# Performance work log

Measured on AMD Instinct MI355X. Metric: run time of the kernel, lower is better.

## Reference

```python
import jax, jax.numpy as jnp
import numpy as np

B, H, W, C = 2, 256, 256, 192
HEADS, WIN, SHIFT = 6, 8, 4
HID = 4 * C
N = WIN * WIN            # tokens per window
HD = C // HEADS
SCALE = HD ** -0.5

# ---- static relative-position index (matches torch buffer construction) ----
_c = np.stack(np.meshgrid(np.arange(WIN), np.arange(WIN), indexing='ij')).reshape(2, -1)
_r = (_c[:, :, None] - _c[:, None, :]).transpose(1, 2, 0)
_r[..., 0] += WIN - 1
_r[..., 1] += WIN - 1
_r[..., 0] *= 2 * WIN - 1
RPI = _r.sum(-1)  # [N, N]

# ---- static shift attention mask (Swin-style region mask, shift_size>0) ----
def _build_shift_mask():
    m = np.zeros((H, W))
    cnt = 0
    sl = (slice(0, -WIN), slice(-WIN, -SHIFT), slice(-SHIFT, None))
    for hs in sl:
        for ws in sl:
            m[hs, ws] = cnt
            cnt += 1
    mw = m.reshape(H // WIN, WIN, W // WIN, WIN).transpose(0, 2, 1, 3).reshape(-1, N)
    am = mw[:, None, :] - mw[:, :, None]  # unsqueeze(1) - unsqueeze(2)
    return jnp.asarray(np.where(am != 0, -100.0, 0.0), jnp.float32)  # [nW, N, N]

ATTN_MASK = _build_shift_mask()

def _win_part(x):  # [B,H,W,c] -> [B*nW, N, c]
    b, c = x.shape[0], x.shape[-1]
    x = x.reshape(b, H // WIN, WIN, W // WIN, WIN, c).transpose(0, 1, 3, 2, 4, 5)
    return x.reshape(-1, N, c)

def _win_rev(w):  # [B*nW, N, c] -> [B,H,W,c]
    c = w.shape[-1]
    x = w.reshape(-1, H // WIN, W // WIN, WIN, WIN, c).transpose(0, 1, 3, 2, 4, 5)
    return x.reshape(-1, H, W, c)

def _ln(x, w, b):
    mu = x.mean(-1, keepdims=True)
    v = ((x - mu) ** 2).mean(-1, keepdims=True)
    return (x - mu) / jnp.sqrt(v + 1e-5) * w + b


def setup_inputs() -> dict:
    key = jax.random.key(0)
    ks = jax.random.split(key, 9)
    s = jnp.float32(0.02)
    f32 = jnp.float32
    return {
        'x': jax.random.normal(ks[0], (B, H * W, C), f32),
        'norm1_w': jnp.ones((C,), f32), 'norm1_b': jnp.zeros((C,), f32),
        'q_w': jax.random.normal(ks[1], (C, C), f32) * s, 'q_b': jnp.zeros((C,), f32),
        'kv_w': jax.random.normal(ks[2], (C, 2 * C), f32) * s, 'kv_b': jnp.zeros((2 * C,), f32),
        'rpb': jax.random.normal(ks[3], ((2 * WIN - 1) ** 2, HEADS), f32) * s,
        'proj_w': jax.random.normal(ks[4], (C, C), f32) * s, 'proj_b': jnp.zeros((C,), f32),
        'norm2_w': jnp.ones((C,), f32), 'norm2_b': jnp.zeros((C,), f32),
        'l1_w': jax.random.normal(ks[5], (C, HID), f32) * s, 'l1_b': jnp.zeros((HID,), f32),
        'dw_w': jax.random.normal(ks[6], (3, 3, 1, HID), f32) * s, 'dw_b': jnp.zeros((HID,), f32),
        'l2_w': jax.random.normal(ks[7], (HID, C), f32) * s, 'l2_b': jnp.zeros((C,), f32),
    }


def reference(x, norm1_w, norm1_b, q_w, q_b, kv_w, kv_b, rpb, proj_w, proj_b,
              norm2_w, norm2_b, l1_w, l1_b, dw_w, dw_b, l2_w, l2_b):
    shortcut = x
    xn = _ln(x, norm1_w, norm1_b)
    q = (xn @ q_w + q_b).reshape(B, H, W, C)
    kv = (xn @ kv_w + kv_b).reshape(B, H, W, 2 * C)
    # cyclic shift
    q = jnp.roll(q, (-SHIFT, -SHIFT), axis=(1, 2))
    kv = jnp.roll(kv, (-SHIFT, -SHIFT), axis=(1, 2))
    # window partition -> heads
    qw = _win_part(q).reshape(-1, N, HEADS, HD).transpose(0, 2, 1, 3)          # [B_,h,N,hd]
    kvw = _win_part(kv).reshape(-1, N, 2, HEADS, HD).transpose(2, 0, 3, 1, 4)
    kw, vw = kvw[0], kvw[1]
    attn = jnp.einsum('bhnd,bhmd->bhnm', qw * SCALE, kw)                       # [B_,h,N,N]
    bias = rpb[RPI.reshape(-1)].reshape(N, N, HEADS).transpose(2, 0, 1)        # [h,N,N]
    attn = attn + bias[None]
    nW = ATTN_MASK.shape[0]
    attn = attn.reshape(B, nW, HEADS, N, N) + ATTN_MASK[None, :, None]
    attn = jax.nn.softmax(attn.reshape(-1, HEADS, N, N), axis=-1)
    y = jnp.einsum('bhnm,bhmd->bnhd', attn, vw).reshape(-1, N, C)
    y = y @ proj_w + proj_b
    xa = _win_rev(y)
    xa = jnp.roll(xa, (SHIFT, SHIFT), axis=(1, 2)).reshape(B, H * W, C)
    x = shortcut + xa
    # LeFF: linear -> GELU -> 3x3 depthwise conv -> GELU -> linear
    xn = _ln(x, norm2_w, norm2_b)
    h = jax.nn.gelu(xn @ l1_w + l1_b, approximate=False).reshape(B, H, W, HID)
    h = jax.lax.conv_general_dilated(h, dw_w, (1, 1), 'SAME',
                                     dimension_numbers=('NHWC', 'HWIO', 'NHWC'),
                                     feature_group_count=HID) + dw_b
    h = jax.nn.gelu(h, approximate=False).reshape(B, H * W, HID)
    return x + (h @ l2_w + l2_b)
```

## Files before the change

kernel.cpp:

```cpp
#include <hip/hip_runtime.h>
#include <math.h>

typedef float f32x4 __attribute__((ext_vector_type(4)));
typedef short bf16x8 __attribute__((ext_vector_type(8)));
typedef short bf16x4 __attribute__((ext_vector_type(4)));

__device__ __forceinline__ short f2bf(float f) {
  unsigned u = __builtin_bit_cast(unsigned, f);
  u = (u + 0x7FFFu + ((u >> 16) & 1u)) >> 16;
  return (short)u;
}
__device__ __forceinline__ float bf2f(short s) {
  unsigned u = ((unsigned)(unsigned short)s) << 16;
  return __builtin_bit_cast(float, u);
}
__device__ __forceinline__ float gelu_exact(float x) {
  return 0.5f * x * (1.0f + erff(x * 0.70710678118654752f));
}
__device__ __forceinline__ void gld16(const short* g, short* l) {
  __builtin_amdgcn_global_load_lds(
      (const __attribute__((address_space(1))) void*)g,
      (__attribute__((address_space(3))) void*)l, 16, 0, 0);
}

__device__ __forceinline__ long perm_row(int b, int ho, int wo) {
  int hs = (ho + 252) & 255, ws = (wo + 252) & 255;
  int w = ((hs >> 3) << 5) | (ws >> 3);
  int t = ((hs & 7) << 3) | (ws & 7);
  return ((long)b << 16) | (w << 6) | t;
}
__device__ __forceinline__ long unperm_row(long m) {
  int b = (int)(m >> 16);
  int w = ((int)m >> 6) & 1023, t = (int)m & 63;
  int hs = ((w >> 5) << 3) | (t >> 3);
  int ws = ((w & 31) << 3) | (t & 7);
  int ho = (hs + 4) & 255, wo = (ws + 4) & 255;
  return ((long)b << 16) | (ho << 8) | wo;
}

__global__ __launch_bounds__(256) void ln1_kernel(const float* __restrict__ x,
                                                  const float* __restrict__ w,
                                                  const float* __restrict__ b,
                                                  short* __restrict__ out) {
  int lane = threadIdx.x & 63;
  long row = (long)blockIdx.x * 4 + (threadIdx.x >> 6);
  const float* xr = x + row * 192;
  float v0 = xr[lane], v1 = xr[lane + 64], v2 = xr[lane + 128];
  float s = v0 + v1 + v2, s2 = v0 * v0 + v1 * v1 + v2 * v2;
#pragma unroll
  for (int m = 1; m < 64; m <<= 1) {
    s += __shfl_xor(s, m);
    s2 += __shfl_xor(s2, m);
  }
  float mu = s * (1.0f / 192.0f);
  float rstd = rsqrtf(s2 * (1.0f / 192.0f) - mu * mu + 1e-5f);
  long drow = perm_row((int)(row >> 16), ((int)row >> 8) & 255, (int)row & 255);
  short* o = out + drow * 192;
  o[lane] = f2bf((v0 - mu) * rstd * w[lane] + b[lane]);
  o[lane + 64] = f2bf((v1 - mu) * rstd * w[lane + 64] + b[lane + 64]);
  o[lane + 128] = f2bf((v2 - mu) * rstd * w[lane + 128] + b[lane + 128]);
}

__global__ __launch_bounds__(256) void ln2_kernel(const short* __restrict__ x,
                                                  const float* __restrict__ w,
                                                  const float* __restrict__ b,
                                                  short* __restrict__ out) {
  int lane = threadIdx.x & 63;
  long row = (long)blockIdx.x * 4 + (threadIdx.x >> 6);
  const short* xr = x + row * 192;
  float v0 = bf2f(xr[lane]), v1 = bf2f(xr[lane + 64]), v2 = bf2f(xr[lane + 128]);
  float s = v0 + v1 + v2, s2 = v0 * v0 + v1 * v1 + v2 * v2;
#pragma unroll
  for (int m = 1; m < 64; m <<= 1) {
    s += __shfl_xor(s, m);
    s2 += __shfl_xor(s2, m);
  }
  float mu = s * (1.0f / 192.0f);
  float rstd = rsqrtf(s2 * (1.0f / 192.0f) - mu * mu + 1e-5f);
  short* o = out + row * 192;
  o[lane] = f2bf((v0 - mu) * rstd * w[lane] + b[lane]);
  o[lane + 64] = f2bf((v1 - mu) * rstd * w[lane + 64] + b[lane + 64]);
  o[lane + 128] = f2bf((v2 - mu) * rstd * w[lane + 128] + b[lane + 128]);
}

__global__ __launch_bounds__(256) void wprep_kernel(const float* __restrict__ w,
                                                    short* __restrict__ bt,
                                                    int K, int N) {
  long i = (long)blockIdx.x * 256 + threadIdx.x;
  if (i >= (long)K * N) return;
  int n = (int)(i / K), k = (int)(i % K);
  bt[i] = f2bf(w[(long)k * N + n]);
}

__global__ __launch_bounds__(256) void bias_prep(const float* __restrict__ rpb,
                                                 float* __restrict__ biasTab) {
  int i = blockIdx.x * 256 + threadIdx.x;
  int k = i & 63, q = (i >> 6) & 63, h = i >> 12;
  int dr = (q >> 3) - (k >> 3) + 7;
  int dc = (q & 7) - (k & 7) + 7;
  biasTab[i] = rpb[(dr * 15 + dc) * 6 + h] * 1.4426950408889634f;
}

__global__ __launch_bounds__(384) void fused_attn_kernel(
    const short* __restrict__ xn, const short* __restrict__ bt1,
    const short* __restrict__ bt2, const float* __restrict__ q_b,
    const float* __restrict__ kv_b, const float* __restrict__ proj_b,
    const float* __restrict__ residf, const float* __restrict__ biasTab,
    short* __restrict__ x2bf) {
  __shared__ short S_[57344];
  const int tid = threadIdx.x;
  const int lane = tid & 63, wid = tid >> 6;
  const int lr = lane & 15, lg = lane >> 4;
  const int bid = blockIdx.x;
  const int wglob = (bid & 7) * 256 + (bid >> 3);
  const int w = wglob & 1023;
  const int wr = w >> 5, wc = w & 31;
  const long wbase = (long)wglob * 64;
  const int RB = 12800 + wid * 7424;

#pragma unroll
  for (int p = 0; p < 4; ++p) {
    int g = p * 384 + tid;
    int r = g / 24, c = g % 24;
    *(float4*)(&S_[r * 200 + c * 8]) =
        *(const float4*)(xn + (wbase + r) * 192 + c * 8);
  }
  __syncthreads();

  {
    f32x4 acc[4][6] = {};
#pragma unroll
    for (int ks = 0; ks < 6; ++ks) {
      bf16x8 a[4], b[6];
#pragma unroll
      for (int mf = 0; mf < 4; ++mf)
        a[mf] = *(const bf16x8*)(&S_[(mf * 16 + lr) * 200 + ks * 32 + lg * 8]);
#pragma unroll
      for (int st = 0; st < 3; ++st)
#pragma unroll
        for (int nf = 0; nf < 2; ++nf)
          b[st * 2 + nf] = *(const bf16x8*)(
              bt1 + (long)(st * 192 + wid * 32 + nf * 16 + lr) * 192 +
              ks * 32 + lg * 8);
#pragma unroll
      for (int mf = 0; mf < 4; ++mf)
#pragma unroll
        for (int j = 0; j < 6; ++j)
          acc[mf][j] = __builtin_amdgcn_mfma_f32_16x16x32_bf16(
              a[mf], b[j], acc[mf][j], 0, 0, 0);
    }
#pragma unroll
    for (int mf = 0; mf < 4; ++mf) {
      int row0 = mf * 16 + lg * 4;
#pragma unroll
      for (int nf = 0; nf < 2; ++nf) {
        int c = nf * 16 + lr;
        float qb = q_b[wid * 32 + c];
        float kb = kv_b[wid * 32 + c];
        float vb = kv_b[192 + wid * 32 + c];
#pragma unroll
        for (int r = 0; r < 4; ++r) {
          S_[RB + (row0 + r) * 40 + c] = f2bf(acc[mf][nf][r] + qb);
          S_[RB + 2560 + (row0 + r) * 40 + c] = f2bf(acc[mf][2 + nf][r] + kb);
        }
        bf16x4 vv;
#pragma unroll
        for (int r = 0; r < 4; ++r) vv[r] = f2bf(acc[mf][4 + nf][r] + vb);
        *(bf16x4*)(&S_[RB + 5120 + c * 72 + row0]) = vv;
      }
    }
  }

  bf16x8 aq[4], bk[4];
#pragma unroll
  for (int i = 0; i < 4; ++i) {
    aq[i] = *(const bf16x8*)(&S_[RB + (i * 16 + lr) * 40 + lg * 8]);
    bk[i] = *(const bf16x8*)(&S_[RB + 2560 + (i * 16 + lr) * 40 + lg * 8]);
  }
  f32x4 s[4][4] = {};
#pragma unroll
  for (int mi = 0; mi < 4; ++mi)
#pragma unroll
    for (int ni = 0; ni < 4; ++ni)
      s[mi][ni] = __builtin_amdgcn_mfma_f32_16x16x32_bf16(aq[mi], bk[ni],
                                                          s[mi][ni], 0, 0, 0);

  const float SCL2 = 0.17677669529663687f * 1.4426950408889634f;
  const float MASKC = -144.26950408889634f;
  const bool edge = (wr == 31) || (wc == 31);
  int ridk[4] = {0, 0, 0, 0};
  if (edge) {
#pragma unroll
    for (int ni = 0; ni < 4; ++ni) {
      int k = ni * 16 + lr;
      int kh = wr * 8 + (k >> 3), kw = wc * 8 + (k & 7);
      ridk[ni] = 3 * ((kh < 248) ? 0 : ((kh < 252) ? 1 : 2)) +
                 ((kw < 248) ? 0 : ((kw < 252) ? 1 : 2));
    }
  }
  float rinv[4][4];
#pragma unroll
  for (int mi = 0; mi < 4; ++mi) {
#pragma unroll
    for (int r = 0; r < 4; ++r) {
      int q = mi * 16 + lg * 4 + r;
      const float* bp = biasTab + (wid << 12) + (q << 6);
      int ridq = 0;
      if (edge) {
        int qh = wr * 8 + (q >> 3), qw = wc * 8 + (q & 7);
        ridq = 3 * ((qh < 248) ? 0 : ((qh < 252) ? 1 : 2)) +
               ((qw < 248) ? 0 : ((qw < 252) ? 1 : 2));
      }
      float lv[4];
      float mx = -1e30f;
#pragma unroll
      for (int ni = 0; ni < 4; ++ni) {
        float lvv = s[mi][ni][r] * SCL2 + bp[ni * 16 + lr];
        if (edge && ridq != ridk[ni]) lvv += MASKC;
        lv[ni] = lvv;
        mx = fmaxf(mx, lvv);
      }
#pragma unroll
      for (int m = 1; m < 16; m <<= 1) mx = fmaxf(mx, __shfl_xor(mx, m));
      float sum = 0.0f;
#pragma unroll
      for (int ni = 0; ni < 4; ++ni) {
        float p = exp2f(lv[ni] - mx);
        lv[ni] = p;
        sum += p;
      }
#pragma unroll
      for (int m = 1; m < 16; m <<= 1) sum += __shfl_xor(sum, m);
      rinv[mi][r] = 1.0f / sum;
#pragma unroll
      for (int ni = 0; ni < 4; ++ni)
        S_[RB + q * 72 + ni * 16 + lr] = f2bf(lv[ni]);
    }
  }

  f32x4 o[4][2] = {};
#pragma unroll
  for (int ks = 0; ks < 2; ++ks) {
    bf16x8 ap[4], bv[2];
#pragma unroll
    for (int mi = 0; mi < 4; ++mi)
      ap[mi] = *(const bf16x8*)(&S_[RB + (mi * 16 + lr) * 72 + ks * 32 +
                                    lg * 8]);
#pragma unroll
    for (int ni = 0; ni < 2; ++ni)
      bv[ni] = *(const bf16x8*)(&S_[RB + 5120 + (ni * 16 + lr) * 72 +
                                    ks * 32 + lg * 8]);
#pragma unroll
    for (int mi = 0; mi < 4; ++mi)
#pragma unroll
      for (int ni = 0; ni < 2; ++ni)
        o[mi][ni] = __builtin_amdgcn_mfma_f32_16x16x32_bf16(ap[mi], bv[ni],
                                                            o[mi][ni], 0, 0, 0);
  }
#pragma unroll
  for (int mi = 0; mi < 4; ++mi)
#pragma unroll
    for (int r = 0; r < 4; ++r) {
      int q = mi * 16 + lg * 4 + r;
      float ri = rinv[mi][r];
#pragma unroll
      for (int ni = 0; ni < 2; ++ni)
        S_[RB + q * 40 + ni * 16 + lr] = f2bf(o[mi][ni][r] * ri);
    }
  __syncthreads();

  {
    f32x4 acc[4][2] = {};
#pragma unroll
    for (int ks = 0; ks < 6; ++ks) {
      bf16x8 a[4], bq[2];
#pragma unroll
      for (int mf = 0; mf < 4; ++mf)
        a[mf] = *(const bf16x8*)(&S_[12800 + ks * 7424 +
                                     (mf * 16 + lr) * 40 + lg * 8]);
#pragma unroll
      for (int nf = 0; nf < 2; ++nf)
        bq[nf] = *(const bf16x8*)(bt2 +
                                  (long)(wid * 32 + nf * 16 + lr) * 192 +
                                  ks * 32 + lg * 8);
#pragma unroll
      for (int mf = 0; mf < 4; ++mf)
#pragma unroll
        for (int nf = 0; nf < 2; ++nf)
          acc[mf][nf] = __builtin_amdgcn_mfma_f32_16x16x32_bf16(
              a[mf], bq[nf], acc[mf][nf], 0, 0, 0);
    }
#pragma unroll
    for (int mf = 0; mf < 4; ++mf)
#pragma unroll
      for (int nf = 0; nf < 2; ++nf) {
        int n = wid * 32 + nf * 16 + lr;
#pragma unroll
        for (int r = 0; r < 4; ++r) {
          long m = wbase + mf * 16 + lg * 4 + r;
          long oidx = unperm_row(m) * 192 + n;
          x2bf[oidx] = f2bf(acc[mf][nf][r] + proj_b[n] + residf[oidx]);
        }
      }
  }
}

template <int NTOT, int EPI>
__global__ __launch_bounds__(256) void gemm1_kernel(
    const short* __restrict__ A, const short* __restrict__ Bt,
    const float* __restrict__ B0, short* __restrict__ outp,
    int nblk, int mgx, int iters, int mtiles) {
  __shared__ short As[128 * 192];
  const int tid = threadIdx.x;
  const int lane = tid & 63, wid = tid >> 6;
  const int lr = lane & 15, lg = lane >> 4;
  const int xcd = blockIdx.x & 7;
  const int i = blockIdx.x >> 3;
  const int n0 = (i % nblk) * 64;
  const int mg = xcd * mgx + i / nblk;

  bf16x8 bf[6][4];
#pragma unroll
  for (int ks = 0; ks < 6; ++ks)
#pragma unroll
    for (int ni = 0; ni < 4; ++ni)
      bf[ks][ni] = *(const bf16x8*)(Bt + (long)(n0 + ni * 16 + lr) * 192 +
                                    ks * 32 + lg * 8);

  int src_s[12];
#pragma unroll
  for (int s = 0; s < 12; ++s) {
    int lo = (wid * 12 + s) * 1024 + lane * 16;
    int r = lo / 384, c = lo % 384;
    src_s[s] = r * 192 + ((c ^ ((r & 7) << 4)) >> 1);
  }
  const int xorv = (lr & 7) << 4;

#pragma unroll 1
  for (int it = 0; it < iters; ++it) {
    int mt = mg * iters + it;
    if (mt >= mtiles) continue;
    long m0 = (long)mt * 128;
    const short* Ab = A + m0 * 192;
    __syncthreads();
#pragma unroll
    for (int s = 0; s < 12; ++s)
      gld16(Ab + src_s[s], As + (wid * 12 + s) * 512);
    __syncthreads();
    f32x4 acc[2][4] = {};
#pragma unroll
    for (int ks = 0; ks < 6; ++ks) {
      const char* asb = (const char*)As;
      const int col = (ks * 64 + lg * 16) ^ xorv;
      bf16x8 a0 = *(const bf16x8*)(asb + (wid * 32 + lr) * 384 + col);
      bf16x8 a1 = *(const bf16x8*)(asb + (wid * 32 + 16 + lr) * 384 + col);
#pragma unroll
      for (int ni = 0; ni < 4; ++ni) {
        acc[0][ni] = __builtin_amdgcn_mfma_f32_16x16x32_bf16(a0, bf[ks][ni],
                                                             acc[0][ni], 0, 0, 0);
        acc[1][ni] = __builtin_amdgcn_mfma_f32_16x16x32_bf16(a1, bf[ks][ni],
                                                             acc[1][ni], 0, 0, 0);
      }
    }
#pragma unroll
    for (int mi = 0; mi < 2; ++mi) {
#pragma unroll
      for (int ni = 0; ni < 4; ++ni) {
        int n = n0 + ni * 16 + lr;
        long rowb = m0 + wid * 32 + mi * 16 + lg * 4;
#pragma unroll
        for (int r = 0; r < 4; ++r) {
          long m = rowb + r;
          outp[m * NTOT + n] = f2bf(gelu_exact(acc[mi][ni][r] + B0[n]));
        }
      }
    }
  }
}

__global__ __launch_bounds__(256) void dwconv_kernel(const short* __restrict__ hbc,
                                                     const float* __restrict__ dww,
                                                     const float* __restrict__ dwb,
                                                     short* __restrict__ h2c,
                                                     int yh) {
  int t = blockIdx.x * 256 + threadIdx.x;
  int cg = t % 96;
  int px = t / 96;
  int strip = blockIdx.y;

  float wv[9][8];
#pragma unroll
  for (int tap = 0; tap < 9; ++tap) {
    float4 a = *(const float4*)(dww + tap * 768 + cg * 8);
    float4 b = *(const float4*)(dww + tap * 768 + cg * 8 + 4);
    wv[tap][0] = a.x; wv[tap][1] = a.y; wv[tap][2] = a.z; wv[tap][3] = a.w;
    wv[tap][4] = b.x; wv[tap][5] = b.y; wv[tap][6] = b.z; wv[tap][7] = b.w;
  }
  float bias[8];
  {
    float4 a = *(const float4*)(dwb + cg * 8);
    float4 b = *(const float4*)(dwb + cg * 8 + 4);
    bias[0] = a.x; bias[1] = a.y; bias[2] = a.z; bias[3] = a.w;
    bias[4] = b.x; bias[5] = b.y; bias[6] = b.z; bias[7] = b.w;
  }

#pragma unroll 2
  for (int pp = 0; pp < 16; ++pp) {
    int py = strip * 16 + pp;
    int ybase = yh * 128 + py;
    float acc[8];
#pragma unroll
    for (int j = 0; j < 8; ++j) acc[j] = bias[j];
#pragma unroll
    for (int dy = 0; dy < 3; ++dy) {
      int yy = ybase + dy - 1;
      if (yy < 0 || yy > 255) continue;
#pragma unroll
      for (int dx = 0; dx < 3; ++dx) {
        int xx = px + dx - 1;
        if (xx < 0 || xx > 255) continue;
        bf16x8 hv = *(const bf16x8*)(hbc + ((long)yy * 256 + xx) * 768 + cg * 8);
#pragma unroll
        for (int j = 0; j < 8; ++j) acc[j] += bf2f(hv[j]) * wv[dy * 3 + dx][j];
      }
    }
    bf16x8 ov;
#pragma unroll
    for (int j = 0; j < 8; ++j) ov[j] = f2bf(gelu_exact(acc[j]));
    *(bf16x8*)(h2c + ((long)py * 256 + px) * 768 + cg * 8) = ov;
  }
}

__global__ __launch_bounds__(256) void gemm2_kernel(
    const short* __restrict__ A, const short* __restrict__ Bt,
    const float* __restrict__ bias, const short* __restrict__ residb,
    float* __restrict__ outp) {
  __shared__ short As[64][72];
  __shared__ short Bs[192][72];
  const int tid = threadIdx.x;
  const int lane = tid & 63, wid = tid >> 6;
  const int lr = lane & 15, lg = lane >> 4;
  const int wm = wid >> 1, wn = wid & 1;
  const int wg = (blockIdx.x & 7) * 64 + (blockIdx.x >> 3);
  const long m0 = (long)wg * 64;

  f32x4 acc[2][6] = {};
#pragma unroll 1
  for (int kc = 0; kc < 12; ++kc) {
    __syncthreads();
#pragma unroll
    for (int p = 0; p < 2; ++p) {
      int g = p * 256 + tid;
      int r = g >> 3, c = g & 7;
      *(float4*)(&As[r][c * 8]) =
          *(const float4*)(A + (m0 + r) * 768 + kc * 64 + c * 8);
    }
#pragma unroll
    for (int p = 0; p < 6; ++p) {
      int g = p * 256 + tid;
      int n = g >> 3, c = g & 7;
      *(float4*)(&Bs[n][c * 8]) =
          *(const float4*)(Bt + (long)n * 768 + kc * 64 + c * 8);
    }
    __syncthreads();
#pragma unroll
    for (int ks = 0; ks < 2; ++ks) {
      bf16x8 a[2], b[6];
#pragma unroll
      for (int mf = 0; mf < 2; ++mf)
        a[mf] = *(const bf16x8*)(&As[wm * 32 + mf * 16 + lr][ks * 32 + lg * 8]);
#pragma unroll
      for (int nf = 0; nf < 6; ++nf)
        b[nf] = *(const bf16x8*)(&Bs[wn * 96 + nf * 16 + lr][ks * 32 + lg * 8]);
#pragma unroll
      for (int mf = 0; mf < 2; ++mf)
#pragma unroll
        for (int nf = 0; nf < 6; ++nf)
          acc[mf][nf] = __builtin_amdgcn_mfma_f32_16x16x32_bf16(
              a[mf], b[nf], acc[mf][nf], 0, 0, 0);
    }
  }
#pragma unroll
  for (int mf = 0; mf < 2; ++mf)
#pragma unroll
    for (int nf = 0; nf < 6; ++nf) {
      int n = wn * 96 + nf * 16 + lr;
      long rowb = m0 + wm * 32 + mf * 16 + lg * 4;
#pragma unroll
      for (int r = 0; r < 4; ++r) {
        long idx = (rowb + r) * 192 + n;
        outp[idx] = acc[mf][nf][r] + bias[n] + bf2f(residb[idx]);
      }
    }
}

extern "C" void kernel_launch(void* const* d_in, const int* in_sizes, int n_in,
                              void* d_out, int out_size, void* d_ws, size_t ws_size,
                              hipStream_t stream) {
  const float* x = (const float*)d_in[0];
  const float* n1w = (const float*)d_in[1];
  const float* n1b = (const float*)d_in[2];
  const float* q_w = (const float*)d_in[3];
  const float* q_b = (const float*)d_in[4];
  const float* kv_w = (const float*)d_in[5];
  const float* kv_b = (const float*)d_in[6];
  const float* rpb = (const float*)d_in[7];
  const float* proj_w = (const float*)d_in[8];
  const float* proj_b = (const float*)d_in[9];
  const float* n2w = (const float*)d_in[10];
  const float* n2b = (const float*)d_in[11];
  const float* l1_w = (const float*)d_in[12];
  const float* l1_b = (const float*)d_in[13];
  const float* dw_w = (const float*)d_in[14];
  const float* dw_b = (const float*)d_in[15];
  const float* l2_w = (const float*)d_in[16];
  const float* l2_b = (const float*)d_in[17];
  float* out = (float*)d_out;

  char* ws = (char*)d_ws;
  short* xn = (short*)ws;
  short* hbc = (short*)(ws + 50331648);
  short* h2c = (short*)(ws + 150994944);
  short* x2bf = (short*)(ws + 201326592);
  short* bt1 = (short*)(ws + 251658240);
  short* bt2 = bt1 + 110592;
  short* bt3 = bt2 + 36864;
  short* bt4 = bt3 + 147456;
  float* biasTab = (float*)(ws + 252542976);
  short* xn2 = xn;

  wprep_kernel<<<144, 256, 0, stream>>>(q_w, bt1, 192, 192);
  wprep_kernel<<<288, 256, 0, stream>>>(kv_w, bt1 + 36864, 192, 384);
  wprep_kernel<<<144, 256, 0, stream>>>(proj_w, bt2, 192, 192);
  wprep_kernel<<<576, 256, 0, stream>>>(l1_w, bt3, 192, 768);
  wprep_kernel<<<576, 256, 0, stream>>>(l2_w, bt4, 768, 192);
  bias_prep<<<96, 256, 0, stream>>>(rpb, biasTab);

  ln1_kernel<<<32768, 256, 0, stream>>>(x, n1w, n1b, xn);
  fused_attn_kernel<<<2048, 384, 0, stream>>>(xn, bt1, bt2, q_b, kv_b, proj_b,
                                              x, biasTab, x2bf);
  ln2_kernel<<<32768, 256, 0, stream>>>(x2bf, n2w, n2b, xn2);

  for (int b = 0; b < 2; ++b) {
    long toff = (long)b * 65536 * 192;
    gemm1_kernel<768, 2><<<1536, 256, 0, stream>>>(
        xn2 + toff, bt3, l1_b, hbc, 12, 16, 4, 512);
    for (int yh = 0; yh < 2; ++yh) {
      long ooff = ((long)b * 65536 + (long)yh * 32768) * 192;
      dwconv_kernel<<<dim3(96, 8), 256, 0, stream>>>(hbc, dw_w, dw_b, h2c, yh);
      gemm2_kernel<<<512, 256, 0, stream>>>(h2c, bt4, l2_b, x2bf + ooff,
                                            out + ooff);
    }
  }
}
```

Baseline: 732.2 us.

## Split attention work across two waves per head and load activations directly

The fused window-attention kernel moves from 6 waves (one per head) to 12 waves: two per head, each owning half the query rows and half the per-head QKV output columns. The projection GEMM is split over 12 waves of 16 columns each. The shared-memory staging of the input tile is dropped, and A fragments are read straight from global memory. This is meant to raise occupancy and latency hiding. In exchange it adds an extra block barrier, larger LDS use per block, and repeated global reads of xn by every wave.

Result: slower. 759.9 us (+3.8%).

```diff
diff --git a/kernel.cpp b/kernel.cpp
--- a/kernel.cpp
+++ b/kernel.cpp
@@ -101,85 +101,75 @@
   biasTab[i] = rpb[(dr * 15 + dc) * 6 + h] * 1.4426950408889634f;
 }
 
-__global__ __launch_bounds__(384) void fused_attn_kernel(
+__global__ __launch_bounds__(768, 3) void fused_attn_kernel(
     const short* __restrict__ xn, const short* __restrict__ bt1,
     const short* __restrict__ bt2, const float* __restrict__ q_b,
     const float* __restrict__ kv_b, const float* __restrict__ proj_b,
     const float* __restrict__ residf, const float* __restrict__ biasTab,
     short* __restrict__ x2bf) {
-  __shared__ short S_[57344];
+  __shared__ short S_[72192];
   const int tid = threadIdx.x;
   const int lane = tid & 63, wid = tid >> 6;
+  const int h = wid >> 1, ha = wid & 1;
   const int lr = lane & 15, lg = lane >> 4;
   const int bid = blockIdx.x;
   const int wglob = (bid & 7) * 256 + (bid >> 3);
   const int w = wglob & 1023;
   const int wr = w >> 5, wc = w & 31;
   const long wbase = (long)wglob * 64;
-  const int RB = 12800 + wid * 7424;
-
-#pragma unroll
-  for (int p = 0; p < 4; ++p) {
-    int g = p * 384 + tid;
-    int r = g / 24, c = g % 24;
-    *(float4*)(&S_[r * 200 + c * 8]) =
-        *(const float4*)(xn + (wbase + r) * 192 + c * 8);
-  }
-  __syncthreads();
+  const int RB = h * 12032;
+  const int cb = h * 32 + ha * 16;
 
   {
-    f32x4 acc[4][6] = {};
+    f32x4 acc[4][3] = {};
 #pragma unroll
     for (int ks = 0; ks < 6; ++ks) {
-      bf16x8 a[4], b[6];
+      bf16x8 a[4], b[3];
 #pragma unroll
       for (int mf = 0; mf < 4; ++mf)
-        a[mf] = *(const bf16x8*)(&S_[(mf * 16 + lr) * 200 + ks * 32 + lg * 8]);
+        a[mf] = *(const bf16x8*)(xn + (wbase + mf * 16 + lr) * 192 +
+                                 ks * 32 + lg * 8);
 #pragma unroll
       for (int st = 0; st < 3; ++st)
-#pragma unroll
-        for (int nf = 0; nf < 2; ++nf)
-          b[st * 2 + nf] = *(const bf16x8*)(
-              bt1 + (long)(st * 192 + wid * 32 + nf * 16 + lr) * 192 +
-              ks * 32 + lg * 8);
+        b[st] = *(const bf16x8*)(bt1 + (long)(st * 192 + cb + lr) * 192 +
+                                 ks * 32 + lg * 8);
 #pragma unroll
       for (int mf = 0; mf < 4; ++mf)
 #pragma unroll
-        for (int j = 0; j < 6; ++j)
-          acc[mf][j] = __builtin_amdgcn_mfma_f32_16x16x32_bf16(
-              a[mf], b[j], acc[mf][j], 0, 0, 0);
-    }
+        for (int st = 0; st < 3; ++st)
+          acc[mf][st] = __builtin_amdgcn_mfma_f32_16x16x32_bf16(
+              a[mf], b[st], acc[mf][st], 0, 0, 0);
+    }
+    const int c2 = ha * 16 + lr;
+    const float qb = q_b[cb + lr];
+    const float kb = kv_b[cb + lr];
+    const float vb = kv_b[192 + cb + lr];
 #pragma unroll
     for (int mf = 0; mf < 4; ++mf) {
       int row0 = mf * 16 + lg * 4;
 #pragma unroll
-      for (int nf = 0; nf < 2; ++nf) {
-        int c = nf * 16 + lr;
-        float qb = q_b[wid * 32 + c];
-        float kb = kv_b[wid * 32 + c];
-        float vb = kv_b[192 + wid * 32 + c];
-#pragma unroll
-        for (int r = 0; r < 4; ++r) {
-          S_[RB + (row0 + r) * 40 + c] = f2bf(acc[mf][nf][r] + qb);
-          S_[RB + 2560 + (row0 + r) * 40 + c] = f2bf(acc[mf][2 + nf][r] + kb);
-        }
-        bf16x4 vv;
-#pragma unroll
-        for (int r = 0; r < 4; ++r) vv[r] = f2bf(acc[mf][4 + nf][r] + vb);
-        *(bf16x4*)(&S_[RB + 5120 + c * 72 + row0]) = vv;
-      }
-    }
-  }
-
-  bf16x8 aq[4], bk[4];
-#pragma unroll
-  for (int i = 0; i < 4; ++i) {
-    aq[i] = *(const bf16x8*)(&S_[RB + (i * 16 + lr) * 40 + lg * 8]);
+      for (int r = 0; r < 4; ++r) {
+        S_[RB + (row0 + r) * 40 + c2] = f2bf(acc[mf][0][r] + qb);
+        S_[RB + 2560 + (row0 + r) * 40 + c2] = f2bf(acc[mf][1][r] + kb);
+      }
+      bf16x4 vv;
+#pragma unroll
+      for (int r = 0; r < 4; ++r) vv[r] = f2bf(acc[mf][2][r] + vb);
+      *(bf16x4*)(&S_[RB + 5120 + c2 * 72 + row0]) = vv;
+    }
+  }
+  __syncthreads();
+
+  bf16x8 aq[2], bk[4];
+#pragma unroll
+  for (int i = 0; i < 2; ++i)
+    aq[i] = *(const bf16x8*)(&S_[RB + (ha * 32 + i * 16 + lr) * 40 + lg * 8]);
+#pragma unroll
+  for (int i = 0; i < 4; ++i)
     bk[i] = *(const bf16x8*)(&S_[RB + 2560 + (i * 16 + lr) * 40 + lg * 8]);
-  }
-  f32x4 s[4][4] = {};
-#pragma unroll
-  for (int mi = 0; mi < 4; ++mi)
+  f32x4 s[2][4] = {};
+#pragma unroll
+  for (int mi = 0; mi < 2; ++mi)
 #pragma unroll
     for (int ni = 0; ni < 4; ++ni)
       s[mi][ni] = __builtin_amdgcn_mfma_f32_16x16x32_bf16(aq[mi], bk[ni],
@@ -198,13 +188,13 @@
                  ((kw < 248) ? 0 : ((kw < 252) ? 1 : 2));
     }
   }
-  float rinv[4][4];
-#pragma unroll
-  for (int mi = 0; mi < 4; ++mi) {
+  float rinv[2][4];
+#pragma unroll
+  for (int mi = 0; mi < 2; ++mi) {
 #pragma unroll
     for (int r = 0; r < 4; ++r) {
-      int q = mi * 16 + lg * 4 + r;
-      const float* bp = biasTab + (wid << 12) + (q << 6);
+      int q = ha * 32 + mi * 16 + lg * 4 + r;
+      const float* bp = biasTab + (h << 12) + (q << 6);
       int ridq = 0;
       if (edge) {
         int qh = wr * 8 + (q >> 3), qw = wc * 8 + (q & 7);
@@ -234,34 +224,35 @@
       rinv[mi][r] = 1.0f / sum;
 #pragma unroll
       for (int ni = 0; ni < 4; ++ni)
-        S_[RB + q * 72 + ni * 16 + lr] = f2bf(lv[ni]);
-    }
-  }
-
-  f32x4 o[4][2] = {};
+        S_[RB + 7424 + q * 72 + ni * 16 + lr] = f2bf(lv[ni]);
+    }
+  }
+
+  f32x4 o[2][2] = {};
 #pragma unroll
   for (int ks = 0; ks < 2; ++ks) {
-    bf16x8 ap[4], bv[2];
-#pragma unroll
-    for (int mi = 0; mi < 4; ++mi)
-      ap[mi] = *(const bf16x8*)(&S_[RB + (mi * 16 + lr) * 72 + ks * 32 +
-                                    lg * 8]);
+    bf16x8 ap[2], bv[2];
+#pragma unroll
+    for (int mi = 0; mi < 2; ++mi)
+      ap[mi] = *(const bf16x8*)(&S_[RB + 7424 +
+                                    (ha * 32 + mi * 16 + lr) * 72 +
+                                    ks * 32 + lg * 8]);
 #pragma unroll
     for (int ni = 0; ni < 2; ++ni)
       bv[ni] = *(const bf16x8*)(&S_[RB + 5120 + (ni * 16 + lr) * 72 +
                                     ks * 32 + lg * 8]);
 #pragma unroll
-    for (int mi = 0; mi < 4; ++mi)
+    for (int mi = 0; mi < 2; ++mi)
 #pragma unroll
       for (int ni = 0; ni < 2; ++ni)
         o[mi][ni] = __builtin_amdgcn_mfma_f32_16x16x32_bf16(ap[mi], bv[ni],
                                                             o[mi][ni], 0, 0, 0);
   }
 #pragma unroll
-  for (int mi = 0; mi < 4; ++mi)
+  for (int mi = 0; mi < 2; ++mi)
 #pragma unroll
     for (int r = 0; r < 4; ++r) {
-      int q = mi * 16 + lg * 4 + r;
+      int q = ha * 32 + mi * 16 + lg * 4 + r;
       float ri = rinv[mi][r];
 #pragma unroll
       for (int ni = 0; ni < 2; ++ni)
@@ -270,37 +261,29 @@
   __syncthreads();
 
   {
-    f32x4 acc[4][2] = {};
+    f32x4 acc[4] = {};
 #pragma unroll
     for (int ks = 0; ks < 6; ++ks) {
-      bf16x8 a[4], bq[2];
+      bf16x8 a[4], bq;
 #pragma unroll
       for (int mf = 0; mf < 4; ++mf)
-        a[mf] = *(const bf16x8*)(&S_[12800 + ks * 7424 +
-                                     (mf * 16 + lr) * 40 + lg * 8]);
-#pragma unroll
-      for (int nf = 0; nf < 2; ++nf)
-        bq[nf] = *(const bf16x8*)(bt2 +
-                                  (long)(wid * 32 + nf * 16 + lr) * 192 +
-                                  ks * 32 + lg * 8);
+        a[mf] = *(const bf16x8*)(&S_[ks * 12032 + (mf * 16 + lr) * 40 +
+                                     lg * 8]);
+      bq = *(const bf16x8*)(bt2 + (long)(wid * 16 + lr) * 192 + ks * 32 +
+                            lg * 8);
 #pragma unroll
       for (int mf = 0; mf < 4; ++mf)
-#pragma unroll
-        for (int nf = 0; nf < 2; ++nf)
-          acc[mf][nf] = __builtin_amdgcn_mfma_f32_16x16x32_bf16(
-              a[mf], bq[nf], acc[mf][nf], 0, 0, 0);
-    }
+        acc[mf] = __builtin_amdgcn_mfma_f32_16x16x32_bf16(a[mf], bq, acc[mf],
+                                                          0, 0, 0);
+    }
+    int n = wid * 16 + lr;
 #pragma unroll
     for (int mf = 0; mf < 4; ++mf)
 #pragma unroll
-      for (int nf = 0; nf < 2; ++nf) {
-        int n = wid * 32 + nf * 16 + lr;
-#pragma unroll
-        for (int r = 0; r < 4; ++r) {
-          long m = wbase + mf * 16 + lg * 4 + r;
-          long oidx = unperm_row(m) * 192 + n;
-          x2bf[oidx] = f2bf(acc[mf][nf][r] + proj_b[n] + residf[oidx]);
-        }
+      for (int r = 0; r < 4; ++r) {
+        long m = wbase + mf * 16 + lg * 4 + r;
+        long oidx = unperm_row(m) * 192 + n;
+        x2bf[oidx] = f2bf(acc[mf][r] + proj_b[n] + residf[oidx]);
       }
   }
 }
@@ -537,7 +520,7 @@
   bias_prep<<<96, 256, 0, stream>>>(rpb, biasTab);
 
   ln1_kernel<<<32768, 256, 0, stream>>>(x, n1w, n1b, xn);
-  fused_attn_kernel<<<2048, 384, 0, stream>>>(xn, bt1, bt2, q_b, kv_b, proj_b,
+  fused_attn_kernel<<<2048, 768, 0, stream>>>(xn, bt1, bt2, q_b, kv_b, proj_b,
                                               x, biasTab, x2bf);
   ln2_kernel<<<32768, 256, 0, stream>>>(x2bf, n2w, n2b, xn2);
 
```

## Make attention kernel persistent over 8 windows with async double-buffered loads

Applied to the files above, without the earlier changes.

The fused attention kernel now runs 256 blocks, each looping over 8 consecutive windows. The next window's normalized input is staged into swizzled LDS through global_load_lds double buffering, and the K/V weight fragments are held in registers across iterations. The residual add and un-permutation move out of the attention epilogue into ln2, which reads the window-ordered output with a gather and writes both x2bf and the normalized tensor. This removes scattered residual reads from the attention kernel and reuses weights across windows. In exchange it needs more LDS and registers, which may lower occupancy, and leaves only 256 blocks to fill the GPU.

After: 862.3 us. +17.8%, slower.

```diff
diff --git a/kernel.cpp b/kernel.cpp
--- a/kernel.cpp
+++ b/kernel.cpp
@@ -28,14 +28,6 @@
   int w = ((hs >> 3) << 5) | (ws >> 3);
   int t = ((hs & 7) << 3) | (ws & 7);
   return ((long)b << 16) | (w << 6) | t;
-}
-__device__ __forceinline__ long unperm_row(long m) {
-  int b = (int)(m >> 16);
-  int w = ((int)m >> 6) & 1023, t = (int)m & 63;
-  int hs = ((w >> 5) << 3) | (t >> 3);
-  int ws = ((w & 31) << 3) | (t & 7);
-  int ho = (hs + 4) & 255, wo = (ws + 4) & 255;
-  return ((long)b << 16) | (ho << 8) | wo;
 }
 
 __global__ __launch_bounds__(256) void ln1_kernel(const float* __restrict__ x,
@@ -61,14 +53,24 @@
   o[lane + 128] = f2bf((v2 - mu) * rstd * w[lane + 128] + b[lane + 128]);
 }
 
-__global__ __launch_bounds__(256) void ln2_kernel(const short* __restrict__ x,
+__global__ __launch_bounds__(256) void ln2_kernel(const float* __restrict__ x,
+                                                  const short* __restrict__ yw,
                                                   const float* __restrict__ w,
                                                   const float* __restrict__ b,
-                                                  short* __restrict__ out) {
+                                                  short* __restrict__ xn2,
+                                                  short* __restrict__ x2bf) {
   int lane = threadIdx.x & 63;
   long row = (long)blockIdx.x * 4 + (threadIdx.x >> 6);
-  const short* xr = x + row * 192;
-  float v0 = bf2f(xr[lane]), v1 = bf2f(xr[lane + 64]), v2 = bf2f(xr[lane + 128]);
+  long drow = perm_row((int)(row >> 16), ((int)row >> 8) & 255, (int)row & 255);
+  const float* xr = x + row * 192;
+  const short* yr = yw + drow * 192;
+  float v0 = xr[lane] + bf2f(yr[lane]);
+  float v1 = xr[lane + 64] + bf2f(yr[lane + 64]);
+  float v2 = xr[lane + 128] + bf2f(yr[lane + 128]);
+  short* xo = x2bf + row * 192;
+  xo[lane] = f2bf(v0);
+  xo[lane + 64] = f2bf(v1);
+  xo[lane + 128] = f2bf(v2);
   float s = v0 + v1 + v2, s2 = v0 * v0 + v1 * v1 + v2 * v2;
 #pragma unroll
   for (int m = 1; m < 64; m <<= 1) {
@@ -77,7 +79,7 @@
   }
   float mu = s * (1.0f / 192.0f);
   float rstd = rsqrtf(s2 * (1.0f / 192.0f) - mu * mu + 1e-5f);
-  short* o = out + row * 192;
+  short* o = xn2 + row * 192;
   o[lane] = f2bf((v0 - mu) * rstd * w[lane] + b[lane]);
   o[lane + 64] = f2bf((v1 - mu) * rstd * w[lane + 64] + b[lane + 64]);
   o[lane + 128] = f2bf((v2 - mu) * rstd * w[lane + 128] + b[lane + 128]);
@@ -105,203 +107,237 @@
     const short* __restrict__ xn, const short* __restrict__ bt1,
     const short* __restrict__ bt2, const float* __restrict__ q_b,
     const float* __restrict__ kv_b, const float* __restrict__ proj_b,
-    const float* __restrict__ residf, const float* __restrict__ biasTab,
-    short* __restrict__ x2bf) {
-  __shared__ short S_[57344];
+    const float* __restrict__ biasTab, short* __restrict__ yw) {
+  __shared__ short S_[69120];
   const int tid = threadIdx.x;
   const int lane = tid & 63, wid = tid >> 6;
   const int lr = lane & 15, lg = lane >> 4;
   const int bid = blockIdx.x;
-  const int wglob = (bid & 7) * 256 + (bid >> 3);
-  const int w = wglob & 1023;
-  const int wr = w >> 5, wc = w & 31;
-  const long wbase = (long)wglob * 64;
-  const int RB = 12800 + wid * 7424;
-
-#pragma unroll
-  for (int p = 0; p < 4; ++p) {
-    int g = p * 384 + tid;
-    int r = g / 24, c = g % 24;
-    *(float4*)(&S_[r * 200 + c * 8]) =
-        *(const float4*)(xn + (wbase + r) * 192 + c * 8);
-  }
-  __syncthreads();
-
-  {
-    f32x4 acc[4][6] = {};
-#pragma unroll
-    for (int ks = 0; ks < 6; ++ks) {
-      bf16x8 a[4], b[6];
+  const int w0 = (bid & 7) * 256 + (bid >> 3) * 8;
+  const int RB = 24576 + wid * 7424;
+
+  bf16x8 bkv[6][2][2];
+#pragma unroll
+  for (int ks = 0; ks < 6; ++ks)
+#pragma unroll
+    for (int st = 1; st < 3; ++st)
+#pragma unroll
+      for (int nf = 0; nf < 2; ++nf)
+        bkv[ks][st - 1][nf] = *(const bf16x8*)(
+            bt1 + (long)(st * 192 + wid * 32 + nf * 16 + lr) * 192 +
+            ks * 32 + lg * 8);
+
+  int src_s[4];
+#pragma unroll
+  for (int s = 0; s < 4; ++s) {
+    int lo = (wid * 4 + s) * 1024 + lane * 16;
+    int r = lo / 384, c = lo % 384;
+    src_s[s] = r * 192 + ((c ^ ((r & 7) << 4)) >> 1);
+  }
+  const int xorv = (lr & 7) << 4;
+
+  auto stage = [&](int buf, int wg) {
+    const short* Ab = xn + (long)wg * 64 * 192;
+#pragma unroll
+    for (int s = 0; s < 4; ++s)
+      gld16(Ab + src_s[s], S_ + buf * 12288 + (wid * 4 + s) * 512);
+  };
+
+  stage(0, w0);
+  int cur = 0;
+
+#pragma unroll 1
+  for (int it = 0; it < 8; ++it) {
+    const int wglob = w0 + it;
+    const int w = wglob & 1023;
+    const int wr = w >> 5, wc = w & 31;
+    const long wbase = (long)wglob * 64;
+    __syncthreads();
+    if (it < 7) stage(cur ^ 1, wglob + 1);
+
+    {
+      f32x4 acc[4][6] = {};
+      const char* asb = (const char*)(S_ + cur * 12288);
+#pragma unroll
+      for (int ks = 0; ks < 6; ++ks) {
+        bf16x8 a[4], bq[2];
+        const int col = (ks * 64 + lg * 16) ^ xorv;
+#pragma unroll
+        for (int mf = 0; mf < 4; ++mf)
+          a[mf] = *(const bf16x8*)(asb + (mf * 16 + lr) * 384 + col);
+#pragma unroll
+        for (int nf = 0; nf < 2; ++nf)
+          bq[nf] = *(const bf16x8*)(bt1 +
+                                    (long)(wid * 32 + nf * 16 + lr) * 192 +
+                                    ks * 32 + lg * 8);
+#pragma unroll
+        for (int mf = 0; mf < 4; ++mf) {
+#pragma unroll
+          for (int nf = 0; nf < 2; ++nf) {
+            acc[mf][nf] = __builtin_amdgcn_mfma_f32_16x16x32_bf16(
+                a[mf], bq[nf], acc[mf][nf], 0, 0, 0);
+            acc[mf][2 + nf] = __builtin_amdgcn_mfma_f32_16x16x32_bf16(
+                a[mf], bkv[ks][0][nf], acc[mf][2 + nf], 0, 0, 0);
+            acc[mf][4 + nf] = __builtin_amdgcn_mfma_f32_16x16x32_bf16(
+                a[mf], bkv[ks][1][nf], acc[mf][4 + nf], 0, 0, 0);
+          }
+        }
+      }
+#pragma unroll
+      for (int mf = 0; mf < 4; ++mf) {
+        int row0 = mf * 16 + lg * 4;
+#pragma unroll
+        for (int nf = 0; nf < 2; ++nf) {
+          int c = nf * 16 + lr;
+          float qb = q_b[wid * 32 + c];
+          float kb = kv_b[wid * 32 + c];
+          float vb = kv_b[192 + wid * 32 + c];
+#pragma unroll
+          for (int r = 0; r < 4; ++r) {
+            S_[RB + (row0 + r) * 40 + c] = f2bf(acc[mf][nf][r] + qb);
+            S_[RB + 2560 + (row0 + r) * 40 + c] = f2bf(acc[mf][2 + nf][r] + kb);
+          }
+          bf16x4 vv;
+#pragma unroll
+          for (int r = 0; r < 4; ++r) vv[r] = f2bf(acc[mf][4 + nf][r] + vb);
+          *(bf16x4*)(&S_[RB + 5120 + c * 72 + row0]) = vv;
+        }
+      }
+    }
+
+    bf16x8 aq[4], bk[4];
+#pragma unroll
+    for (int i = 0; i < 4; ++i) {
+      aq[i] = *(const bf16x8*)(&S_[RB + (i * 16 + lr) * 40 + lg * 8]);
+      bk[i] = *(const bf16x8*)(&S_[RB + 2560 + (i * 16 + lr) * 40 + lg * 8]);
+    }
+    f32x4 s[4][4] = {};
+#pragma unroll
+    for (int mi = 0; mi < 4; ++mi)
+#pragma unroll
+      for (int ni = 0; ni < 4; ++ni)
+        s[mi][ni] = __builtin_amdgcn_mfma_f32_16x16x32_bf16(aq[mi], bk[ni],
+                                                            s[mi][ni], 0, 0, 0);
+
+    const float SCL2 = 0.17677669529663687f * 1.4426950408889634f;
+    const float MASKC = -144.26950408889634f;
+    const bool edge = (wr == 31) || (wc == 31);
+    int ridk[4] = {0, 0, 0, 0};
+    if (edge) {
+#pragma unroll
+      for (int ni = 0; ni < 4; ++ni) {
+        int k = ni * 16 + lr;
+        int kh = wr * 8 + (k >> 3), kw = wc * 8 + (k & 7);
+        ridk[ni] = 3 * ((kh < 248) ? 0 : ((kh < 252) ? 1 : 2)) +
+                   ((kw < 248) ? 0 : ((kw < 252) ? 1 : 2));
+      }
+    }
+    float rinv[4][4];
+#pragma unroll
+    for (int mi = 0; mi < 4; ++mi) {
+#pragma unroll
+      for (int r = 0; r < 4; ++r) {
+        int q = mi * 16 + lg * 4 + r;
+        const float* bp = biasTab + (wid << 12) + (q << 6);
+        int ridq = 0;
+        if (edge) {
+          int qh = wr * 8 + (q >> 3), qw = wc * 8 + (q & 7);
+          ridq = 3 * ((qh < 248) ? 0 : ((qh < 252) ? 1 : 2)) +
+                 ((qw < 248) ? 0 : ((qw < 252) ? 1 : 2));
+        }
+        float lv[4];
+        float mx = -1e30f;
+#pragma unroll
+        for (int ni = 0; ni < 4; ++ni) {
+          float lvv = s[mi][ni][r] * SCL2 + bp[ni * 16 + lr];
+          if (edge && ridq != ridk[ni]) lvv += MASKC;
+          lv[ni] = lvv;
+          mx = fmaxf(mx, lvv);
+        }
+#pragma unroll
+        for (int m = 1; m < 16; m <<= 1) mx = fmaxf(mx, __shfl_xor(mx, m));
+        float sum = 0.0f;
+#pragma unroll
+        for (int ni = 0; ni < 4; ++ni) {
+          float p = exp2f(lv[ni] - mx);
+          lv[ni] = p;
+          sum += p;
+        }
+#pragma unroll
+        for (int m = 1; m < 16; m <<= 1) sum += __shfl_xor(sum, m);
+        rinv[mi][r] = 1.0f / sum;
+#pragma unroll
+        for (int ni = 0; ni < 4; ++ni)
+          S_[RB + q * 72 + ni * 16 + lr] = f2bf(lv[ni]);
+      }
+    }
+
+    f32x4 o[4][2] = {};
+#pragma unroll
+    for (int ks = 0; ks < 2; ++ks) {
+      bf16x8 ap[4], bv[2];
+#pragma unroll
+      for (int mi = 0; mi < 4; ++mi)
+        ap[mi] = *(const bf16x8*)(&S_[RB + (mi * 16 + lr) * 72 + ks * 32 +
+                                      lg * 8]);
+#pragma unroll
+      for (int ni = 0; ni < 2; ++ni)
+        bv[ni] = *(const bf16x8*)(&S_[RB + 5120 + (ni * 16 + lr) * 72 +
+                                      ks * 32 + lg * 8]);
+#pragma unroll
+      for (int mi = 0; mi < 4; ++mi)
+#pragma unroll
+        for (int ni = 0; ni < 2; ++ni)
+          o[mi][ni] = __builtin_amdgcn_mfma_f32_16x16x32_bf16(
+              ap[mi], bv[ni], o[mi][ni], 0, 0, 0);
+    }
+#pragma unroll
+    for (int mi = 0; mi < 4; ++mi)
+#pragma unroll
+      for (int r = 0; r < 4; ++r) {
+        int q = mi * 16 + lg * 4 + r;
+        float ri = rinv[mi][r];
+#pragma unroll
+        for (int ni = 0; ni < 2; ++ni)
+          S_[RB + q * 40 + ni * 16 + lr] = f2bf(o[mi][ni][r] * ri);
+      }
+    __syncthreads();
+
+    {
+      f32x4 acc[4][2] = {};
+#pragma unroll
+      for (int ks = 0; ks < 6; ++ks) {
+        bf16x8 a[4], bq[2];
+#pragma unroll
+        for (int mf = 0; mf < 4; ++mf)
+          a[mf] = *(const bf16x8*)(&S_[24576 + ks * 7424 +
+                                       (mf * 16 + lr) * 40 + lg * 8]);
+#pragma unroll
+        for (int nf = 0; nf < 2; ++nf)
+          bq[nf] = *(const bf16x8*)(bt2 +
+                                    (long)(wid * 32 + nf * 16 + lr) * 192 +
+                                    ks * 32 + lg * 8);
+#pragma unroll
+        for (int mf = 0; mf < 4; ++mf)
+#pragma unroll
+          for (int nf = 0; nf < 2; ++nf)
+            acc[mf][nf] = __builtin_amdgcn_mfma_f32_16x16x32_bf16(
+                a[mf], bq[nf], acc[mf][nf], 0, 0, 0);
+      }
 #pragma unroll
       for (int mf = 0; mf < 4; ++mf)
-        a[mf] = *(const bf16x8*)(&S_[(mf * 16 + lr) * 200 + ks * 32 + lg * 8]);
-#pragma unroll
-      for (int st = 0; st < 3; ++st)
-#pragma unroll
-        for (int nf = 0; nf < 2; ++nf)
-          b[st * 2 + nf] = *(const bf16x8*)(
-              bt1 + (long)(st * 192 + wid * 32 + nf * 16 + lr) * 192 +
-              ks * 32 + lg * 8);
-#pragma unroll
-      for (int mf = 0; mf < 4; ++mf)
-#pragma unroll
-        for (int j = 0; j < 6; ++j)
-          acc[mf][j] = __builtin_amdgcn_mfma_f32_16x16x32_bf16(
-              a[mf], b[j], acc[mf][j], 0, 0, 0);
-    }
-#pragma unroll
-    for (int mf = 0; mf < 4; ++mf) {
-      int row0 = mf * 16 + lg * 4;
-#pragma unroll
-      for (int nf = 0; nf < 2; ++nf) {
-        int c = nf * 16 + lr;
-        float qb = q_b[wid * 32 + c];
-        float kb = kv_b[wid * 32 + c];
-        float vb = kv_b[192 + wid * 32 + c];
-#pragma unroll
-        for (int r = 0; r < 4; ++r) {
-          S_[RB + (row0 + r) * 40 + c] = f2bf(acc[mf][nf][r] + qb);
-          S_[RB + 2560 + (row0 + r) * 40 + c] = f2bf(acc[mf][2 + nf][r] + kb);
-        }
-        bf16x4 vv;
-#pragma unroll
-        for (int r = 0; r < 4; ++r) vv[r] = f2bf(acc[mf][4 + nf][r] + vb);
-        *(bf16x4*)(&S_[RB + 5120 + c * 72 + row0]) = vv;
-      }
-    }
-  }
-
-  bf16x8 aq[4], bk[4];
-#pragma unroll
-  for (int i = 0; i < 4; ++i) {
-    aq[i] = *(const bf16x8*)(&S_[RB + (i * 16 + lr) * 40 + lg * 8]);
-    bk[i] = *(const bf16x8*)(&S_[RB + 2560 + (i * 16 + lr) * 40 + lg * 8]);
-  }
-  f32x4 s[4][4] = {};
-#pragma unroll
-  for (int mi = 0; mi < 4; ++mi)
-#pragma unroll
-    for (int ni = 0; ni < 4; ++ni)
-      s[mi][ni] = __builtin_amdgcn_mfma_f32_16x16x32_bf16(aq[mi], bk[ni],
-                                                          s[mi][ni], 0, 0, 0);
-
-  const float SCL2 = 0.17677669529663687f * 1.4426950408889634f;
-  const float MASKC = -144.26950408889634f;
-  const bool edge = (wr == 31) || (wc == 31);
-  int ridk[4] = {0, 0, 0, 0};
-  if (edge) {
-#pragma unroll
-    for (int ni = 0; ni < 4; ++ni) {
-      int k = ni * 16 + lr;
-      int kh = wr * 8 + (k >> 3), kw = wc * 8 + (k & 7);
-      ridk[ni] = 3 * ((kh < 248) ? 0 : ((kh < 252) ? 1 : 2)) +
-                 ((kw < 248) ? 0 : ((kw < 252) ? 1 : 2));
-    }
-  }
-  float rinv[4][4];
-#pragma unroll
-  for (int mi = 0; mi < 4; ++mi) {
-#pragma unroll
-    for (int r = 0; r < 4; ++r) {
-      int q = mi * 16 + lg * 4 + r;
-      const float* bp = biasTab + (wid << 12) + (q << 6);
-      int ridq = 0;
-      if (edge) {
-        int qh = wr * 8 + (q >> 3), qw = wc * 8 + (q & 7);
-        ridq = 3 * ((qh < 248) ? 0 : ((qh < 252) ? 1 : 2)) +
-               ((qw < 248) ? 0 : ((qw < 252) ? 1 : 2));
-      }
-      float lv[4];
-      float mx = -1e30f;
-#pragma unroll
-      for (int ni = 0; ni < 4; ++ni) {
-        float lvv = s[mi][ni][r] * SCL2 + bp[ni * 16 + lr];
-        if (edge && ridq != ridk[ni]) lvv += MASKC;
-        lv[ni] = lvv;
-        mx = fmaxf(mx, lvv);
-      }
-#pragma unroll
-      for (int m = 1; m < 16; m <<= 1) mx = fmaxf(mx, __shfl_xor(mx, m));
-      float sum = 0.0f;
-#pragma unroll
-      for (int ni = 0; ni < 4; ++ni) {
-        float p = exp2f(lv[ni] - mx);
-        lv[ni] = p;
-        sum += p;
-      }
-#pragma unroll
-      for (int m = 1; m < 16; m <<= 1) sum += __shfl_xor(sum, m);
-      rinv[mi][r] = 1.0f / sum;
-#pragma unroll
-      for (int ni = 0; ni < 4; ++ni)
-        S_[RB + q * 72 + ni * 16 + lr] = f2bf(lv[ni]);
-    }
-  }
-
-  f32x4 o[4][2] = {};
-#pragma unroll
-  for (int ks = 0; ks < 2; ++ks) {
-    bf16x8 ap[4], bv[2];
-#pragma unroll
-    for (int mi = 0; mi < 4; ++mi)
-      ap[mi] = *(const bf16x8*)(&S_[RB + (mi * 16 + lr) * 72 + ks * 32 +
-                                    lg * 8]);
-#pragma unroll
-    for (int ni = 0; ni < 2; ++ni)
-      bv[ni] = *(const bf16x8*)(&S_[RB + 5120 + (ni * 16 + lr) * 72 +
-                                    ks * 32 + lg * 8]);
-#pragma unroll
-    for (int mi = 0; mi < 4; ++mi)
-#pragma unroll
-      for (int ni = 0; ni < 2; ++ni)
-        o[mi][ni] = __builtin_amdgcn_mfma_f32_16x16x32_bf16(ap[mi], bv[ni],
-                                                            o[mi][ni], 0, 0, 0);
-  }
-#pragma unroll
-  for (int mi = 0; mi < 4; ++mi)
-#pragma unroll
-    for (int r = 0; r < 4; ++r) {
-      int q = mi * 16 + lg * 4 + r;
-      float ri = rinv[mi][r];
-#pragma unroll
-      for (int ni = 0; ni < 2; ++ni)
-        S_[RB + q * 40 + ni * 16 + lr] = f2bf(o[mi][ni][r] * ri);
-    }
-  __syncthreads();
-
-  {
-    f32x4 acc[4][2] = {};
-#pragma unroll
-    for (int ks = 0; ks < 6; ++ks) {
-      bf16x8 a[4], bq[2];
-#pragma unroll
-      for (int mf = 0; mf < 4; ++mf)
-        a[mf] = *(const bf16x8*)(&S_[12800 + ks * 7424 +
-                                     (mf * 16 + lr) * 40 + lg * 8]);
-#pragma unroll
-      for (int nf = 0; nf < 2; ++nf)
-        bq[nf] = *(const bf16x8*)(bt2 +
-                                  (long)(wid * 32 + nf * 16 + lr) * 192 +
-                                  ks * 32 + lg * 8);
-#pragma unroll
-      for (int mf = 0; mf < 4; ++mf)
-#pragma unroll
-        for (int nf = 0; nf < 2; ++nf)
-          acc[mf][nf] = __builtin_amdgcn_mfma_f32_16x16x32_bf16(
-              a[mf], bq[nf], acc[mf][nf], 0, 0, 0);
-    }
-#pragma unroll
-    for (int mf = 0; mf < 4; ++mf)
-#pragma unroll
-      for (int nf = 0; nf < 2; ++nf) {
-        int n = wid * 32 + nf * 16 + lr;
-#pragma unroll
-        for (int r = 0; r < 4; ++r) {
-          long m = wbase + mf * 16 + lg * 4 + r;
-          long oidx = unperm_row(m) * 192 + n;
-          x2bf[oidx] = f2bf(acc[mf][nf][r] + proj_b[n] + residf[oidx]);
-        }
-      }
+#pragma unroll
+        for (int nf = 0; nf < 2; ++nf) {
+          int n = wid * 32 + nf * 16 + lr;
+          float pb = proj_b[n];
+#pragma unroll
+          for (int r = 0; r < 4; ++r) {
+            long m = wbase + mf * 16 + lg * 4 + r;
+            yw[m * 192 + n] = f2bf(acc[mf][nf][r] + pb);
+          }
+        }
+    }
+    cur ^= 1;
   }
 }
 
@@ -520,7 +556,7 @@
   char* ws = (char*)d_ws;
   short* xn = (short*)ws;
   short* hbc = (short*)(ws + 50331648);
-  short* h2c = (short*)(ws + 150994944);
+  short* yw = (short*)(ws + 150994944);
   short* x2bf = (short*)(ws + 201326592);
   short* bt1 = (short*)(ws + 251658240);
   short* bt2 = bt1 + 110592;
@@ -528,6 +564,7 @@
   short* bt4 = bt3 + 147456;
   float* biasTab = (float*)(ws + 252542976);
   short* xn2 = xn;
+  short* h2c = yw;
 
   wprep_kernel<<<144, 256, 0, stream>>>(q_w, bt1, 192, 192);
   wprep_kernel<<<288, 256, 0, stream>>>(kv_w, bt1 + 36864, 192, 384);
@@ -537,9 +574,9 @@
   bias_prep<<<96, 256, 0, stream>>>(rpb, biasTab);
 
   ln1_kernel<<<32768, 256, 0, stream>>>(x, n1w, n1b, xn);
-  fused_attn_kernel<<<2048, 384, 0, stream>>>(xn, bt1, bt2, q_b, kv_b, proj_b,
-                                              x, biasTab, x2bf);
-  ln2_kernel<<<32768, 256, 0, stream>>>(x2bf, n2w, n2b, xn2);
+  fused_attn_kernel<<<256, 384, 0, stream>>>(xn, bt1, bt2, q_b, kv_b, proj_b,
+                                             biasTab, yw);
+  ln2_kernel<<<32768, 256, 0, stream>>>(x, yw, n2w, n2b, xn2, x2bf);
 
   for (int b = 0; b < 2; ++b) {
     long toff = (long)b * 65536 * 192;
```
